# Performance work log

Measured on AMD Instinct MI355X. Metric: run time of the kernel, lower is better.

The kernel has to match this reference:

```python
import jax, jax.numpy as jnp
import numpy as np

N_NODES = 100000
N_EDGES = 1600000
D = 128
K = 3
LEAKY_ALPHA = 0.2  # tf.nn.leaky_relu default
L2_EPS = 1e-12     # tf.math.l2_normalize default


def spmm(row, col, val, x, n_nodes):
    # y[r] = sum_{e: row[e]==r} val[e] * x[col[e]]
    return jax.ops.segment_sum(val[:, None] * x[col], row, num_segments=n_nodes)


def setup_inputs() -> dict:
    key = jax.random.key(0)
    ks = jax.random.split(key, 8)
    embeddings = jax.random.normal(ks[0], (N_NODES, D), dtype=jnp.float32) * 0.1
    edge_row = jax.random.randint(ks[1], (N_EDGES,), 0, N_NODES, dtype=jnp.int32)
    edge_col = jax.random.randint(ks[2], (N_EDGES,), 0, N_NODES, dtype=jnp.int32)
    # normalized-laplacian-like positive weights
    edge_val = jax.random.uniform(ks[3], (N_EDGES,), dtype=jnp.float32) * 0.05
    W_gc = jax.random.normal(ks[4], (K, D, D), dtype=jnp.float32) * (1.0 / np.sqrt(D))
    b_gc = jax.random.normal(ks[5], (K, D), dtype=jnp.float32) * 0.01
    W_bi = jax.random.normal(ks[6], (K, D, D), dtype=jnp.float32) * (1.0 / np.sqrt(D))
    b_bi = jax.random.normal(ks[7], (K, D), dtype=jnp.float32) * 0.01
    return {"embeddings": embeddings, "edge_row": edge_row, "edge_col": edge_col,
            "edge_val": edge_val, "W_gc": W_gc, "b_gc": b_gc, "W_bi": W_bi, "b_bi": b_bi}


def reference(embeddings, edge_row, edge_col, edge_val, W_gc, b_gc, W_bi, b_bi):
    n = embeddings.shape[0]
    x = embeddings
    depth_embeddings = [x]
    for i in range(W_gc.shape[0]):
        Lx = spmm(edge_row, edge_col, edge_val, x, n)   # L @ x  (L has zero diag)
        prop = Lx + x                                    # S @ x, S = L with diag 1
        emb = prop @ W_gc[i] + b_gc[i][None, :]
        bi = (x * Lx) @ W_bi[i] + b_bi[i][None, :]
        x = jax.nn.leaky_relu(emb + bi, negative_slope=LEAKY_ALPHA)
        sq = jnp.sum(x * x, axis=1, keepdims=True)
        norm_x = x / jnp.sqrt(jnp.maximum(sq, L2_EPS))   # tf l2_normalize semantics
        depth_embeddings.append(norm_x)
        x = norm_x  # note: original feeds normalized x to next layer via loop var? see notes
    return jnp.concatenate(depth_embeddings, axis=1)  # [N, (K+1)*D]
```

## Files before the change

kernel.cpp:

```cpp
#include <hip/hip_runtime.h>
#include <hip/hip_bf16.h>

#define ND 128
#define LDO 512
#define ALPHA 0.2f
#define L2EPS 1e-12f
#define SCAN_B 256
#define NCHUNK 256
#define RPB 512

typedef __attribute__((ext_vector_type(8))) short short8;
typedef __attribute__((ext_vector_type(4))) float f32x4;
typedef __attribute__((ext_vector_type(2))) float f32x2;

__device__ __forceinline__ short f2bf(float f) {
    union { float f; unsigned u; } c; c.f = f;
    unsigned u = c.u;
    unsigned r = (u + 0x7fffu + ((u >> 16) & 1u)) >> 16;
    return (short)r;
}
__device__ __forceinline__ float bf2f(unsigned short u) {
    union { unsigned u; float f; } c; c.u = ((unsigned)u) << 16;
    return c.f;
}
__device__ __forceinline__ void gload_lds16(const void* g, void* l) {
    __builtin_amdgcn_global_load_lds(
        (const __attribute__((address_space(1))) unsigned int*)g,
        (__attribute__((address_space(3))) unsigned int*)l, 16, 0, 0);
}

__global__ void copy_emb_kernel(const float* __restrict__ emb, float* __restrict__ out,
                                unsigned short* __restrict__ xb,
                                unsigned int* __restrict__ xf8w, int n) {
    int idx = blockIdx.x * blockDim.x + threadIdx.x;
    int total = n * 32;
    if (idx >= total) return;
    int r = idx >> 5, c4 = idx & 31;
    const float4 v = *reinterpret_cast<const float4*>(emb + (size_t)r * ND + c4 * 4);
    *reinterpret_cast<float4*>(out + (size_t)r * LDO + c4 * 4) = v;
    ushort4 b;
    b.x = (unsigned short)f2bf(v.x); b.y = (unsigned short)f2bf(v.y);
    b.z = (unsigned short)f2bf(v.z); b.w = (unsigned short)f2bf(v.w);
    *reinterpret_cast<ushort4*>(xb + (size_t)r * ND + c4 * 4) = b;
    unsigned int u = __builtin_amdgcn_cvt_pk_fp8_f32(v.x, v.y, 0, false);
    u = __builtin_amdgcn_cvt_pk_fp8_f32(v.z, v.w, u, true);
    xf8w[(size_t)r * 32 + c4] = u;
}

__global__ __launch_bounds__(256) void bucket_hist_kernel(const int* __restrict__ erow,
                                                          int* __restrict__ gcnt,
                                                          int n_edges, int nb, int ch) {
    __shared__ int cnt[256];
    int b = blockIdx.x;
    cnt[threadIdx.x] = 0;
    __syncthreads();
    int s = b * ch, e = min(n_edges, s + ch);
    for (int j = s + threadIdx.x; j < e; j += 256) {
        atomicAdd(&cnt[erow[j] >> 9], 1);
    }
    __syncthreads();
    for (int i = threadIdx.x; i < nb; i += 256) gcnt[i * NCHUNK + b] = cnt[i];
}

__global__ __launch_bounds__(SCAN_B) void scanA_kernel(const int* __restrict__ in,
                                                       int* __restrict__ outp,
                                                       int* __restrict__ partials, int n) {
    __shared__ int sm[SCAN_B];
    int i = blockIdx.x * SCAN_B + threadIdx.x;
    int v = (i < n) ? in[i] : 0;
    sm[threadIdx.x] = v;
    __syncthreads();
#pragma unroll
    for (int off = 1; off < SCAN_B; off <<= 1) {
        int t = (threadIdx.x >= off) ? sm[threadIdx.x - off] : 0;
        __syncthreads();
        sm[threadIdx.x] += t;
        __syncthreads();
    }
    if (i < n) outp[i] = sm[threadIdx.x] - v;
    if (threadIdx.x == SCAN_B - 1) partials[blockIdx.x] = sm[SCAN_B - 1];
}

__global__ __launch_bounds__(512) void scanB_kernel(int* __restrict__ partials, int nb) {
    __shared__ int sm[512];
    int v = (threadIdx.x < nb) ? partials[threadIdx.x] : 0;
    sm[threadIdx.x] = v;
    __syncthreads();
#pragma unroll
    for (int off = 1; off < 512; off <<= 1) {
        int t = (threadIdx.x >= off) ? sm[threadIdx.x - off] : 0;
        __syncthreads();
        sm[threadIdx.x] += t;
        __syncthreads();
    }
    if (threadIdx.x < nb) partials[threadIdx.x] = sm[threadIdx.x] - v;
}

__global__ void scan_add_kernel(int* __restrict__ arr, const int* __restrict__ partials, int n) {
    int i = blockIdx.x * blockDim.x + threadIdx.x;
    if (i < n) arr[i] += partials[i >> 8];
}

__global__ __launch_bounds__(256) void bucket_scatter_kernel(const int* __restrict__ erow,
                                                             const int* __restrict__ ecol,
                                                             const float* __restrict__ eval,
                                                             const int* __restrict__ gbase,
                                                             int2* __restrict__ tmp,
                                                             int n_edges, int nb, int ch) {
    __shared__ int cur[256];
    int b = blockIdx.x;
    for (int i = threadIdx.x; i < nb; i += 256) cur[i] = gbase[i * NCHUNK + b];
    __syncthreads();
    int s = b * ch, e = min(n_edges, s + ch);
    for (int j = s + threadIdx.x; j < e; j += 256) {
        int r = erow[j];
        int pos = atomicAdd(&cur[r >> 9], 1);
        int2 p;
        p.x = ecol[j] | ((r & (RPB - 1)) << 17);
        p.y = __float_as_int(eval[j]);
        tmp[pos] = p;
    }
}

__global__ __launch_bounds__(256) void bucket_sort_kernel(const int2* __restrict__ tmp,
                                                          const int* __restrict__ gbase,
                                                          int2* __restrict__ pv,
                                                          int* __restrict__ row_start,
                                                          int n, int n_edges, int nb) {
    __shared__ int hist[RPB];
    __shared__ int cur[RPB];
    __shared__ int sc[256];
    const int t = threadIdx.x;
    const int bkt = blockIdx.x;
    const int r0 = bkt << 9;
    const int s = gbase[bkt * NCHUNK];
    const int e = (bkt + 1 < nb) ? gbase[(bkt + 1) * NCHUNK] : n_edges;

    for (int i = t; i < RPB; i += 256) hist[i] = 0;
    __syncthreads();
    for (int j = s + t; j < e; j += 256) atomicAdd(&hist[tmp[j].x >> 17], 1);
    __syncthreads();
    int a0 = hist[2 * t], a1 = hist[2 * t + 1];
    sc[t] = a0 + a1;
    __syncthreads();
#pragma unroll
    for (int off = 1; off < 256; off <<= 1) {
        int v = (t >= off) ? sc[t - off] : 0;
        __syncthreads();
        sc[t] += v;
        __syncthreads();
    }
    int base = s + sc[t] - a0 - a1;
    cur[2 * t] = base;
    cur[2 * t + 1] = base + a0;
    __syncthreads();
    int r1 = min(n, r0 + RPB);
    for (int i = t; i < r1 - r0; i += 256) row_start[r0 + i] = cur[i];
    if (t == 0 && r1 == n) row_start[n] = n_edges;
    __syncthreads();
    for (int j = s + t; j < e; j += 256) {
        int2 p = tmp[j];
        int pos = atomicAdd(&cur[p.x >> 17], 1);
        int2 q;
        q.x = p.x & 0x1FFFF;
        q.y = p.y;
        pv[pos] = q;
    }
}

__global__ __launch_bounds__(256) void spmm_axm_kernel(const int* __restrict__ row_start,
                                                       const int2* __restrict__ pv,
                                                       const unsigned char* __restrict__ xf8,
                                                       const unsigned short* __restrict__ xb,
                                                       unsigned short* __restrict__ Axm, int n) {
    int r = blockIdx.x * 16 + (threadIdx.x >> 4);
    if (r >= n) return;
    int l = threadIdx.x & 15;
    int s = row_start[r], e = row_start[r + 1];
    float a[8] = {0.f, 0.f, 0.f, 0.f, 0.f, 0.f, 0.f, 0.f};
    int j = s;
    for (; j + 1 < e; j += 2) {
        int2 p0 = pv[j], p1 = pv[j + 1];
        float v0 = __int_as_float(p0.y), v1 = __int_as_float(p1.y);
        uint2 q0 = *reinterpret_cast<const uint2*>(xf8 + (size_t)p0.x * ND + l * 8);
        uint2 q1 = *reinterpret_cast<const uint2*>(xf8 + (size_t)p1.x * ND + l * 8);
        f32x2 g0 = __builtin_amdgcn_cvt_pk_f32_fp8(q0.x, false);
        f32x2 g1 = __builtin_amdgcn_cvt_pk_f32_fp8(q0.x, true);
        f32x2 g2 = __builtin_amdgcn_cvt_pk_f32_fp8(q0.y, false);
        f32x2 g3 = __builtin_amdgcn_cvt_pk_f32_fp8(q0.y, true);
        f32x2 h0 = __builtin_amdgcn_cvt_pk_f32_fp8(q1.x, false);
        f32x2 h1 = __builtin_amdgcn_cvt_pk_f32_fp8(q1.x, true);
        f32x2 h2 = __builtin_amdgcn_cvt_pk_f32_fp8(q1.y, false);
        f32x2 h3 = __builtin_amdgcn_cvt_pk_f32_fp8(q1.y, true);
        a[0] += v0 * g0.x + v1 * h0.x;
        a[1] += v0 * g0.y + v1 * h0.y;
        a[2] += v0 * g1.x + v1 * h1.x;
        a[3] += v0 * g1.y + v1 * h1.y;
        a[4] += v0 * g2.x + v1 * h2.x;
        a[5] += v0 * g2.y + v1 * h2.y;
        a[6] += v0 * g3.x + v1 * h3.x;
        a[7] += v0 * g3.y + v1 * h3.y;
    }
    if (j < e) {
        int2 p0 = pv[j];
        float v0 = __int_as_float(p0.y);
        uint2 q0 = *reinterpret_cast<const uint2*>(xf8 + (size_t)p0.x * ND + l * 8);
        f32x2 g0 = __builtin_amdgcn_cvt_pk_f32_fp8(q0.x, false);
        f32x2 g1 = __builtin_amdgcn_cvt_pk_f32_fp8(q0.x, true);
        f32x2 g2 = __builtin_amdgcn_cvt_pk_f32_fp8(q0.y, false);
        f32x2 g3 = __builtin_amdgcn_cvt_pk_f32_fp8(q0.y, true);
        a[0] += v0 * g0.x; a[1] += v0 * g0.y;
        a[2] += v0 * g1.x; a[3] += v0 * g1.y;
        a[4] += v0 * g2.x; a[5] += v0 * g2.y;
        a[6] += v0 * g3.x; a[7] += v0 * g3.y;
    }
    short8 xv = *reinterpret_cast<const short8*>(xb + (size_t)r * ND + l * 8);
    short8 prv, xmv;
#pragma unroll
    for (int q = 0; q < 8; ++q) {
        float xf = bf2f((unsigned short)xv[q]);
        prv[q] = f2bf(xf + a[q]);
        xmv[q] = f2bf(xf * a[q]);
    }
    int sz = r & 7;
    unsigned short* rowp = Axm + (size_t)r * 256;
    *reinterpret_cast<short8*>(rowp + ((l        ^ sz) << 3)) = prv;
    *reinterpret_cast<short8*>(rowp + (((16 + l) ^ sz) << 3)) = xmv;
}

__global__ void prep_w_kernel(const float* __restrict__ Wgc, const float* __restrict__ bgc,
                              const float* __restrict__ Wbi, const float* __restrict__ bbi,
                              short* __restrict__ Wt2, float* __restrict__ bsum) {
    int z = blockIdx.x;
    int k = blockIdx.y;
    int t = threadIdx.x;
    int nn = t & 127;
    int h  = (t < 128) ? 0 : 1;
    const float* src = h ? (Wbi + ((size_t)z * 128 + k) * 128)
                         : (Wgc + ((size_t)z * 128 + k) * 128);
    float v = src[nn];
    int idx16 = k >> 3, e8 = k & 7;
    size_t addr = ((size_t)(z * 2 + h) * 128 + nn) * 128 + ((idx16 ^ (nn & 7)) << 3) + e8;
    Wt2[addr] = f2bf(v);
    if (k == 0 && t < 128) bsum[z * 128 + t] = bgc[z * 128 + t] + bbi[z * 128 + t];
}

__global__ __launch_bounds__(256) void fused_layer_mfma(
        const unsigned short* __restrict__ Axm,
        const short* __restrict__ Wt2,
        const float* __restrict__ bsum,
        float* __restrict__ xout,
        unsigned short* __restrict__ xbout,
        unsigned char* __restrict__ xf8out,
        int n) {
    __shared__ short A_lds[64 * 256];
    __shared__ short W_lds[128 * 128];

    const int tid  = threadIdx.x;
    const int row0 = blockIdx.x * 64;
    const int lane = tid & 63;
    const int w    = tid >> 6;
    const int lrow = lane & 15;
    const int kgrp = lane >> 4;

    {
        const char* gA = (const char*)(Axm + (size_t)row0 * 256) + w * 8192 + lane * 16;
        char*       lA = (char*)A_lds + w * 8192;
        const char* gW = (const char*)Wt2 + w * 8192 + lane * 16;
        char*       lW = (char*)W_lds + w * 8192;
#pragma unroll
        for (int it = 0; it < 8; ++it) {
            gload_lds16(gA + it * 1024, lA + it * 1024);
            gload_lds16(gW + it * 1024, lW + it * 1024);
        }
    }
    asm volatile("s_waitcnt vmcnt(0)" ::: "memory");
    __syncthreads();

    f32x4 acc[8];
#pragma unroll
    for (int nf = 0; nf < 8; ++nf) acc[nf] = (f32x4){0.f, 0.f, 0.f, 0.f};

    const int ar  = w * 16 + lrow;
    const int as_ = ar & 7;

#pragma unroll
    for (int ksl = 0; ksl < 4; ++ksl) {
        int kkl = ksl * 4 + kgrp;
        short8 af = *reinterpret_cast<const short8*>(&A_lds[ar * 256 + ((kkl ^ as_) << 3)]);
#pragma unroll
        for (int nf = 0; nf < 8; ++nf) {
            int nr = nf * 16 + lrow;
            short8 bfr = *reinterpret_cast<const short8*>(&W_lds[nr * 128 + ((kkl ^ (nr & 7)) << 3)]);
            acc[nf] = __builtin_amdgcn_mfma_f32_16x16x32_bf16(af, bfr, acc[nf], 0, 0, 0);
        }
    }
    __syncthreads();
    {
        const char* gW = (const char*)Wt2 + 32768 + w * 8192 + lane * 16;
        char*       lW = (char*)W_lds + w * 8192;
#pragma unroll
        for (int it = 0; it < 8; ++it) gload_lds16(gW + it * 1024, lW + it * 1024);
    }
    asm volatile("s_waitcnt vmcnt(0)" ::: "memory");
    __syncthreads();

#pragma unroll
    for (int ksl = 0; ksl < 4; ++ksl) {
        int kkl = ksl * 4 + kgrp;
        short8 af = *reinterpret_cast<const short8*>(&A_lds[ar * 256 + (((16 + kkl) ^ as_) << 3)]);
#pragma unroll
        for (int nf = 0; nf < 8; ++nf) {
            int nr = nf * 16 + lrow;
            short8 bfr = *reinterpret_cast<const short8*>(&W_lds[nr * 128 + ((kkl ^ (nr & 7)) << 3)]);
            acc[nf] = __builtin_amdgcn_mfma_f32_16x16x32_bf16(af, bfr, acc[nf], 0, 0, 0);
        }
    }

    float bsv[8];
#pragma unroll
    for (int nf = 0; nf < 8; ++nf) bsv[nf] = bsum[nf * 16 + lrow];

#pragma unroll
    for (int reg = 0; reg < 4; ++reg) {
        int grow = row0 + w * 16 + kgrp * 4 + reg;
        float v[8];
        float ssq = 0.f;
#pragma unroll
        for (int nf = 0; nf < 8; ++nf) {
            float tv = acc[nf][reg] + bsv[nf];
            tv = tv > 0.f ? tv : ALPHA * tv;
            v[nf] = tv;
            ssq += tv * tv;
        }
        ssq += __shfl_xor(ssq, 1);
        ssq += __shfl_xor(ssq, 2);
        ssq += __shfl_xor(ssq, 4);
        ssq += __shfl_xor(ssq, 8);
        float sc = 1.0f / sqrtf(fmaxf(ssq, L2EPS));
        if (grow < n) {
            float* op = xout + (size_t)grow * LDO;
            unsigned short* bp = xbout + (size_t)grow * ND;
            unsigned char* fp = xf8out + (size_t)grow * ND;
#pragma unroll
            for (int nf = 0; nf < 8; ++nf) {
                float ov = v[nf] * sc;
                op[nf * 16 + lrow] = ov;
                bp[nf * 16 + lrow] = (unsigned short)f2bf(ov);
                unsigned int u8 = __builtin_amdgcn_cvt_pk_fp8_f32(ov, ov, 0, false);
                fp[nf * 16 + lrow] = (unsigned char)(u8 & 0xff);
            }
        }
    }
}

extern "C" void kernel_launch(void* const* d_in, const int* in_sizes, int n_in,
                              void* d_out, int out_size, void* d_ws, size_t ws_size,
                              hipStream_t stream) {
    const float* emb  = (const float*)d_in[0];
    const int*   erow = (const int*)d_in[1];
    const int*   ecol = (const int*)d_in[2];
    const float* eval = (const float*)d_in[3];
    const float* Wgc  = (const float*)d_in[4];
    const float* bgc  = (const float*)d_in[5];
    const float* Wbi  = (const float*)d_in[6];
    const float* bbi  = (const float*)d_in[7];
    float* out = (float*)d_out;

    const int n        = in_sizes[0] / ND;
    const int n_edges  = in_sizes[1];
    const int n_layers = in_sizes[5] / ND;

    const int nb = (n + RPB - 1) >> 9;
    const int ch = (n_edges + NCHUNK - 1) / NCHUNK;
    const int ng = nb * NCHUNK;

    char* ws = (char*)d_ws;
    size_t off = 0;
    auto alloc = [&](size_t bytes) { void* p = ws + off; off = (off + bytes + 255) & ~(size_t)255; return p; };
    unsigned short* xb  = (unsigned short*)alloc((size_t)n * ND * sizeof(short));
    unsigned char*  xf8 = (unsigned char*) alloc((size_t)n * ND);
    unsigned short* Axm = (unsigned short*)alloc((size_t)(n + 64) * 256 * sizeof(short));
    int2*  pv        = (int2*) alloc((size_t)n_edges * sizeof(int2));
    int2*  tmp       = (int2*) alloc((size_t)n_edges * sizeof(int2));
    int*   row_start = (int*)  alloc((size_t)(n + 1) * sizeof(int));
    int*   gcnt      = (int*)  alloc((size_t)ng * sizeof(int));
    int*   gbase     = (int*)  alloc((size_t)ng * sizeof(int));
    int*   partials  = (int*)  alloc(512 * sizeof(int));
    short* Wt2       = (short*)alloc((size_t)n_layers * 2 * 128 * 128 * sizeof(short));
    float* bsum      = (float*)alloc((size_t)n_layers * 128 * sizeof(float));
    (void)ws_size;

    {
        int total = n * 32;
        copy_emb_kernel<<<(total + 255) / 256, 256, 0, stream>>>(emb, out, xb,
                                                                 (unsigned int*)xf8, n);
    }

    {
        dim3 g(n_layers, 128);
        prep_w_kernel<<<g, 256, 0, stream>>>(Wgc, bgc, Wbi, bbi, Wt2, bsum);
    }

    bucket_hist_kernel<<<NCHUNK, 256, 0, stream>>>(erow, gcnt, n_edges, nb, ch);
    {
        int nblk = (ng + SCAN_B - 1) / SCAN_B;
        scanA_kernel<<<nblk, SCAN_B, 0, stream>>>(gcnt, gbase, partials, ng);
        scanB_kernel<<<1, 512, 0, stream>>>(partials, nblk);
        scan_add_kernel<<<(ng + 255) / 256, 256, 0, stream>>>(gbase, partials, ng);
    }
    bucket_scatter_kernel<<<NCHUNK, 256, 0, stream>>>(erow, ecol, eval, gbase, tmp, n_edges, nb, ch);
    bucket_sort_kernel<<<nb, 256, 0, stream>>>(tmp, gbase, pv, row_start, n, n_edges, nb);

    for (int i = 0; i < n_layers; ++i) {
        spmm_axm_kernel<<<(n + 15) / 16, 256, 0, stream>>>(row_start, pv, xf8, xb, Axm, n);
        fused_layer_mfma<<<(n + 63) / 64, 256, 0, stream>>>(
            Axm, Wt2 + (size_t)i * 2 * 128 * 128, bsum + (size_t)i * 128,
            out + (size_t)(i + 1) * ND, xb, xf8, n);
    }
}
```

Before: 355.6 us.

## Fold scan fixup into consumers, unroll SpMM gathers by four, nontemporal output stores

Removes the scan_add kernel launch by having the bucket scatter and sort kernels add the per-block partial offset themselves when reading the scanned counts. Unrolls the SpMM edge loop from two to four edges so more independent fp8 row gathers are in flight per thread. Writes the fp32 output with nontemporal stores so the streaming output pollutes the cache less. The extra unrolling raises register use and the remainder loop now iterates up to three times.

```diff
diff --git a/kernel.cpp b/kernel.cpp
--- a/kernel.cpp
+++ b/kernel.cpp
@@ -96,20 +96,17 @@
     if (threadIdx.x < nb) partials[threadIdx.x] = sm[threadIdx.x] - v;
 }
 
-__global__ void scan_add_kernel(int* __restrict__ arr, const int* __restrict__ partials, int n) {
-    int i = blockIdx.x * blockDim.x + threadIdx.x;
-    if (i < n) arr[i] += partials[i >> 8];
-}
-
 __global__ __launch_bounds__(256) void bucket_scatter_kernel(const int* __restrict__ erow,
                                                              const int* __restrict__ ecol,
                                                              const float* __restrict__ eval,
-                                                             const int* __restrict__ gbase,
+                                                             const int* __restrict__ gscan,
+                                                             const int* __restrict__ part,
                                                              int2* __restrict__ tmp,
                                                              int n_edges, int nb, int ch) {
     __shared__ int cur[256];
     int b = blockIdx.x;
-    for (int i = threadIdx.x; i < nb; i += 256) cur[i] = gbase[i * NCHUNK + b];
+    for (int i = threadIdx.x; i < nb; i += 256)
+        cur[i] = gscan[i * NCHUNK + b] + part[i];
     __syncthreads();
     int s = b * ch, e = min(n_edges, s + ch);
     for (int j = s + threadIdx.x; j < e; j += 256) {
@@ -123,7 +120,8 @@
 }
 
 __global__ __launch_bounds__(256) void bucket_sort_kernel(const int2* __restrict__ tmp,
-                                                          const int* __restrict__ gbase,
+                                                          const int* __restrict__ gscan,
+                                                          const int* __restrict__ part,
                                                           int2* __restrict__ pv,
                                                           int* __restrict__ row_start,
                                                           int n, int n_edges, int nb) {
@@ -133,8 +131,8 @@
     const int t = threadIdx.x;
     const int bkt = blockIdx.x;
     const int r0 = bkt << 9;
-    const int s = gbase[bkt * NCHUNK];
-    const int e = (bkt + 1 < nb) ? gbase[(bkt + 1) * NCHUNK] : n_edges;
+    const int s = gscan[bkt * NCHUNK] + part[bkt];
+    const int e = (bkt + 1 < nb) ? (gscan[(bkt + 1) * NCHUNK] + part[bkt + 1]) : n_edges;
 
     for (int i = t; i < RPB; i += 256) hist[i] = 0;
     __syncthreads();
@@ -179,29 +177,40 @@
     int s = row_start[r], e = row_start[r + 1];
     float a[8] = {0.f, 0.f, 0.f, 0.f, 0.f, 0.f, 0.f, 0.f};
     int j = s;
-    for (; j + 1 < e; j += 2) {
-        int2 p0 = pv[j], p1 = pv[j + 1];
-        float v0 = __int_as_float(p0.y), v1 = __int_as_float(p1.y);
+    for (; j + 3 < e; j += 4) {
+        int2 p0 = pv[j], p1 = pv[j + 1], p2 = pv[j + 2], p3 = pv[j + 3];
         uint2 q0 = *reinterpret_cast<const uint2*>(xf8 + (size_t)p0.x * ND + l * 8);
         uint2 q1 = *reinterpret_cast<const uint2*>(xf8 + (size_t)p1.x * ND + l * 8);
+        uint2 q2 = *reinterpret_cast<const uint2*>(xf8 + (size_t)p2.x * ND + l * 8);
+        uint2 q3 = *reinterpret_cast<const uint2*>(xf8 + (size_t)p3.x * ND + l * 8);
+        float v0 = __int_as_float(p0.y), v1 = __int_as_float(p1.y);
+        float v2 = __int_as_float(p2.y), v3 = __int_as_float(p3.y);
         f32x2 g0 = __builtin_amdgcn_cvt_pk_f32_fp8(q0.x, false);
         f32x2 g1 = __builtin_amdgcn_cvt_pk_f32_fp8(q0.x, true);
         f32x2 g2 = __builtin_amdgcn_cvt_pk_f32_fp8(q0.y, false);
         f32x2 g3 = __builtin_amdgcn_cvt_pk_f32_fp8(q0.y, true);
-        f32x2 h0 = __builtin_amdgcn_cvt_pk_f32_fp8(q1.x, false);
-        f32x2 h1 = __builtin_amdgcn_cvt_pk_f32_fp8(q1.x, true);
-        f32x2 h2 = __builtin_amdgcn_cvt_pk_f32_fp8(q1.y, false);
-        f32x2 h3 = __builtin_amdgcn_cvt_pk_f32_fp8(q1.y, true);
-        a[0] += v0 * g0.x + v1 * h0.x;
-        a[1] += v0 * g0.y + v1 * h0.y;
-        a[2] += v0 * g1.x + v1 * h1.x;
-        a[3] += v0 * g1.y + v1 * h1.y;
-        a[4] += v0 * g2.x + v1 * h2.x;
-        a[5] += v0 * g2.y + v1 * h2.y;
-        a[6] += v0 * g3.x + v1 * h3.x;
-        a[7] += v0 * g3.y + v1 * h3.y;
-    }
-    if (j < e) {
+        a[0] += v0 * g0.x; a[1] += v0 * g0.y; a[2] += v0 * g1.x; a[3] += v0 * g1.y;
+        a[4] += v0 * g2.x; a[5] += v0 * g2.y; a[6] += v0 * g3.x; a[7] += v0 * g3.y;
+        g0 = __builtin_amdgcn_cvt_pk_f32_fp8(q1.x, false);
+        g1 = __builtin_amdgcn_cvt_pk_f32_fp8(q1.x, true);
+        g2 = __builtin_amdgcn_cvt_pk_f32_fp8(q1.y, false);
+        g3 = __builtin_amdgcn_cvt_pk_f32_fp8(q1.y, true);
+        a[0] += v1 * g0.x; a[1] += v1 * g0.y; a[2] += v1 * g1.x; a[3] += v1 * g1.y;
+        a[4] += v1 * g2.x; a[5] += v1 * g2.y; a[6] += v1 * g3.x; a[7] += v1 * g3.y;
+        g0 = __builtin_amdgcn_cvt_pk_f32_fp8(q2.x, false);
+        g1 = __builtin_amdgcn_cvt_pk_f32_fp8(q2.x, true);
+        g2 = __builtin_amdgcn_cvt_pk_f32_fp8(q2.y, false);
+        g3 = __builtin_amdgcn_cvt_pk_f32_fp8(q2.y, true);
+        a[0] += v2 * g0.x; a[1] += v2 * g0.y; a[2] += v2 * g1.x; a[3] += v2 * g1.y;
+        a[4] += v2 * g2.x; a[5] += v2 * g2.y; a[6] += v2 * g3.x; a[7] += v2 * g3.y;
+        g0 = __builtin_amdgcn_cvt_pk_f32_fp8(q3.x, false);
+        g1 = __builtin_amdgcn_cvt_pk_f32_fp8(q3.x, true);
+        g2 = __builtin_amdgcn_cvt_pk_f32_fp8(q3.y, false);
+        g3 = __builtin_amdgcn_cvt_pk_f32_fp8(q3.y, true);
+        a[0] += v3 * g0.x; a[1] += v3 * g0.y; a[2] += v3 * g1.x; a[3] += v3 * g1.y;
+        a[4] += v3 * g2.x; a[5] += v3 * g2.y; a[6] += v3 * g3.x; a[7] += v3 * g3.y;
+    }
+    for (; j < e; ++j) {
         int2 p0 = pv[j];
         float v0 = __int_as_float(p0.y);
         uint2 q0 = *reinterpret_cast<const uint2*>(xf8 + (size_t)p0.x * ND + l * 8);
@@ -345,7 +354,7 @@
 #pragma unroll
             for (int nf = 0; nf < 8; ++nf) {
                 float ov = v[nf] * sc;
-                op[nf * 16 + lrow] = ov;
+                __builtin_nontemporal_store(ov, op + nf * 16 + lrow);
                 bp[nf * 16 + lrow] = (unsigned short)f2bf(ov);
                 unsigned int u8 = __builtin_amdgcn_cvt_pk_fp8_f32(ov, ov, 0, false);
                 fp[nf * 16 + lrow] = (unsigned char)(u8 & 0xff);
@@ -385,7 +394,7 @@
     int2*  tmp       = (int2*) alloc((size_t)n_edges * sizeof(int2));
     int*   row_start = (int*)  alloc((size_t)(n + 1) * sizeof(int));
     int*   gcnt      = (int*)  alloc((size_t)ng * sizeof(int));
-    int*   gbase     = (int*)  alloc((size_t)ng * sizeof(int));
+    int*   gscan     = (int*)  alloc((size_t)ng * sizeof(int));
     int*   partials  = (int*)  alloc(512 * sizeof(int));
     short* Wt2       = (short*)alloc((size_t)n_layers * 2 * 128 * 128 * sizeof(short));
     float* bsum      = (float*)alloc((size_t)n_layers * 128 * sizeof(float));
@@ -405,12 +414,13 @@
     bucket_hist_kernel<<<NCHUNK, 256, 0, stream>>>(erow, gcnt, n_edges, nb, ch);
     {
         int nblk = (ng + SCAN_B - 1) / SCAN_B;
-        scanA_kernel<<<nblk, SCAN_B, 0, stream>>>(gcnt, gbase, partials, ng);
+        scanA_kernel<<<nblk, SCAN_B, 0, stream>>>(gcnt, gscan, partials, ng);
         scanB_kernel<<<1, 512, 0, stream>>>(partials, nblk);
-        scan_add_kernel<<<(ng + 255) / 256, 256, 0, stream>>>(gbase, partials, ng);
-    }
-    bucket_scatter_kernel<<<NCHUNK, 256, 0, stream>>>(erow, ecol, eval, gbase, tmp, n_edges, nb, ch);
-    bucket_sort_kernel<<<nb, 256, 0, stream>>>(tmp, gbase, pv, row_start, n, n_edges, nb);
+    }
+    bucket_scatter_kernel<<<NCHUNK, 256, 0, stream>>>(erow, ecol, eval, gscan, partials,
+                                                      tmp, n_edges, nb, ch);
+    bucket_sort_kernel<<<nb, 256, 0, stream>>>(tmp, gscan, partials, pv, row_start,
+                                               n, n_edges, nb);
 
     for (int i = 0; i < n_layers; ++i) {
         spmm_axm_kernel<<<(n + 15) / 16, 256, 0, stream>>>(row_start, pv, xf8, xb, Axm, n);
```

Result: faster. 328.6 us (-7.6%).
